# Kernel optimization log

Hardware: AMD Instinct MI355X
Metric: run time of the kernel (lower is better)

Reference implementation:

```python
import jax, jax.numpy as jnp
import numpy as np

B, S, H, G, DH = 2, 2048, 16, 4, 64
D = H * DH        # 1024
DKV = G * DH      # 256
SCALE = 1.0 / np.sqrt(DH).astype(np.float32)


def apply_rope(x, rope):
    # x: [..., S, DH]; rope: [2, S, DH] (rope[0]=cos, rope[1]=sin)
    xr = x.reshape(*x.shape[:-1], DH // 2, 2)
    x_rot = jnp.stack([-xr[..., 1], xr[..., 0]], axis=-1).reshape(x.shape)
    return x * rope[0] + x_rot * rope[1]


def setup_inputs() -> dict:
    key = jax.random.key(0)
    ks = jax.random.split(key, 5)
    X = jax.random.normal(ks[0], (B, S, D), dtype=jnp.float32)
    Wq = jax.random.normal(ks[1], (D, D), dtype=jnp.float32) / np.sqrt(D).astype(np.float32)
    Wk = jax.random.normal(ks[2], (DKV, D), dtype=jnp.float32) / np.sqrt(D).astype(np.float32)
    Wv = jax.random.normal(ks[3], (DKV, D), dtype=jnp.float32) / np.sqrt(D).astype(np.float32)
    Wo = jax.random.normal(ks[4], (D, D), dtype=jnp.float32) / np.sqrt(D).astype(np.float32)
    # standard RoPE angles, interleaved (pairs (0,1),(2,3),...)
    pos = jnp.arange(S, dtype=jnp.float32)
    inv_freq = 1.0 / (10000.0 ** (jnp.arange(0, DH, 2, dtype=jnp.float32) / DH))
    ang = pos[:, None] * inv_freq[None, :]          # [S, DH/2]
    ang = jnp.repeat(ang, 2, axis=-1)               # [S, DH]
    rope = jnp.stack([jnp.cos(ang), jnp.sin(ang)])  # [2, S, DH]
    causal = jnp.tril(jnp.ones((S, S), dtype=bool))
    return {"X": X, "Wq": Wq, "Wk": Wk, "Wv": Wv, "Wo": Wo, "rope": rope, "causal": causal}


def reference(X, Wq, Wk, Wv, Wo, rope, causal):
    # QKV projections (torch Linear: y = x @ W.T)
    Q = (X @ Wq.T).reshape(B, S, H, DH).transpose(0, 2, 1, 3)   # [B,H,S,DH]
    K = (X @ Wk.T).reshape(B, S, G, DH).transpose(0, 2, 1, 3)   # [B,G,S,DH]
    V = (X @ Wv.T).reshape(B, S, G, DH).transpose(0, 2, 1, 3)   # [B,G,S,DH]
    Q = apply_rope(Q, rope)
    K = apply_rope(K, rope)
    # GQA: repeat KV heads (repeat_interleave semantics)
    K = jnp.repeat(K, H // G, axis=1)                            # [B,H,S,DH]
    V = jnp.repeat(V, H // G, axis=1)
    scores = SCALE * jnp.einsum('bhqd,bhkd->bhqk', Q, K)         # [B,H,S,S]
    scores = jnp.where(causal, scores, -jnp.inf)
    A = jax.nn.softmax(scores, axis=-1)
    Y = jnp.einsum('bhqk,bhkd->bhqd', A, V)                      # [B,H,S,DH]
    Y = Y.transpose(0, 2, 1, 3).reshape(B, S, D)
    return Y @ Wo.T
```

## Files before the change

### kernel.cpp

```cpp
#include <hip/hip_runtime.h>
#include <hip/hip_bf16.h>

#define B_   2
#define S_   2048
#define H_   16
#define G_   4
#define DH_  64
#define D_   1024
#define DKV_ 256
#define SCALE_ 0.125f
#define LDQK_ 1280

using short8  = __attribute__((ext_vector_type(8))) short;
using floatx4 = __attribute__((ext_vector_type(4))) float;
typedef unsigned short ushort_t;

__device__ __forceinline__ ushort_t f2bf(float f) {
    union { float f; unsigned u; } v; v.f = f;
    unsigned r = v.u + 0x7fffu + ((v.u >> 16) & 1u);
    return (ushort_t)(r >> 16);
}
__device__ __forceinline__ unsigned cvt_pk_bf16(float lo, float hi) {
    unsigned r;
    asm("v_cvt_pk_bf16_f32 %0, %1, %2" : "=v"(r) : "v"(lo), "v"(hi));
    return r;
}

__device__ __forceinline__ void gload16(const ushort_t* g, ushort_t* l) {
    __builtin_amdgcn_global_load_lds(
        (const __attribute__((address_space(1))) void*)g,
        (__attribute__((address_space(3))) void*)l, 16, 0, 0);
}

__global__ void pack_all(const float* __restrict__ X,  const float* __restrict__ Wq,
                         const float* __restrict__ Wk, const float* __restrict__ Wv,
                         const float* __restrict__ Wo, ushort_t* __restrict__ dst) {
    const int X4  = B_ * S_ * D_ / 4;
    const int QW4 = D_ * D_ / 4;
    const int KW4 = DKV_ * D_ / 4;
    int i = blockIdx.x * blockDim.x + threadIdx.x;
    const float* src; int off;
    if (i < X4)                        { src = X;  off = i; }
    else if (i < X4 + QW4)             { src = Wq; off = i - X4; }
    else if (i < X4 + QW4 + KW4)       { src = Wk; off = i - X4 - QW4; }
    else if (i < X4 + QW4 + 2 * KW4)   { src = Wv; off = i - X4 - QW4 - KW4; }
    else                               { src = Wo; off = i - X4 - QW4 - 2 * KW4; }
    float4 v = reinterpret_cast<const float4*>(src)[off];
    ushort4 o;
    o.x = f2bf(v.x); o.y = f2bf(v.y); o.z = f2bf(v.z); o.w = f2bf(v.w);
    reinterpret_cast<ushort4*>(dst)[i] = o;
}

__global__ __launch_bounds__(256)
void gemm_all(int mode,
              const ushort_t* __restrict__ Xb,  const ushort_t* __restrict__ Wqkb,
              const ushort_t* __restrict__ Wvb, const ushort_t* __restrict__ Wob,
              ushort_t* __restrict__ QKb, ushort_t* __restrict__ Vtb,
              const ushort_t* __restrict__ Yb, float* __restrict__ Cout,
              const float* __restrict__ rope, float qscale)
{
    __shared__ __align__(16) ushort_t Asm[2][128 * 64];
    __shared__ __align__(16) ushort_t Bsm[2][128 * 64];

    const ushort_t *Aorig, *Borig;
    ushort_t* Cb = nullptr; float* Cf = nullptr;
    int m0, n0, ldc, epi;
    if (mode == 1) {
        m0 = blockIdx.x * 128; n0 = blockIdx.y * 128;
        Aorig = Yb; Borig = Wob; Cf = Cout; ldc = D_; epi = 1;
    } else {
        const int bx = blockIdx.x;
        if (bx < 320) {
            m0 = (bx / 10) * 128; n0 = (bx % 10) * 128;
            Aorig = Xb; Borig = Wqkb; Cb = QKb; ldc = LDQK_; epi = 2;
        } else {
            const int idx = bx - 320, b = idx >> 5, rem = idx & 31;
            m0 = (rem >> 4) * 128; n0 = (rem & 15) * 128;
            Aorig = Wvb; Borig = Xb + (long)b * S_ * D_;
            Cb = Vtb + (long)b * DKV_ * S_; ldc = S_; epi = 0;
        }
    }

    const int tid = threadIdx.x, l = tid & 63, w = tid >> 6;
    const int wr = (w >> 1) * 64, wc = (w & 1) * 64;
    const int lr = l & 15, lkb = l >> 4;

    const int srow = w * 8 + (l >> 3);
    const int scol = ((l & 7) ^ ((l >> 3) & 7)) * 8;
    const ushort_t* Ast = Aorig + (long)(m0 + srow) * D_ + scol;
    const ushort_t* Bst = Borig + (long)(n0 + srow) * D_ + scol;

#define GSTAGE(buf, kt)                                                    \
    {                                                                      \
        _Pragma("unroll")                                                  \
        for (int rr = 0; rr < 4; ++rr) {                                   \
            gload16(Ast + (long)rr * 32 * D_ + (kt), &Asm[buf][w * 512 + rr * 2048]); \
            gload16(Bst + (long)rr * 32 * D_ + (kt), &Bsm[buf][w * 512 + rr * 2048]); \
        }                                                                  \
    }

    floatx4 acc[4][4] = {};
    const int xr = (lr & 7) << 4;
    GSTAGE(0, 0);
    for (int i = 0; i < 16; ++i) {
        const int cur = i & 1;
        if (i < 15) {
            GSTAGE(cur ^ 1, (i + 1) * 64);
            asm volatile("s_waitcnt vmcnt(8)" ::: "memory");
        } else {
            asm volatile("s_waitcnt vmcnt(0)" ::: "memory");
        }
        __builtin_amdgcn_s_barrier();

#pragma unroll
        for (int ks = 0; ks < 2; ++ks) {
            short8 a[4], bb[4];
#pragma unroll
            for (int ii = 0; ii < 4; ++ii) {
                const int row = wr + ii * 16 + lr;
                a[ii] = *(const short8*)&Asm[cur][(row * 128 + ((ks * 64 + lkb * 16) ^ xr)) >> 1];
            }
#pragma unroll
            for (int j = 0; j < 4; ++j) {
                const int row = wc + j * 16 + lr;
                bb[j] = *(const short8*)&Bsm[cur][(row * 128 + ((ks * 64 + lkb * 16) ^ xr)) >> 1];
            }
            __builtin_amdgcn_s_setprio(1);
#pragma unroll
            for (int ii = 0; ii < 4; ++ii)
#pragma unroll
                for (int j = 0; j < 4; ++j)
                    acc[ii][j] = __builtin_amdgcn_mfma_f32_16x16x32_bf16(a[ii], bb[j], acc[ii][j], 0, 0, 0);
            __builtin_amdgcn_s_setprio(0);
        }
        __builtin_amdgcn_s_barrier();
    }
#undef GSTAGE

    const int rrow = lkb * 4;
#pragma unroll
    for (int i = 0; i < 4; ++i) {
#pragma unroll
        for (int j = 0; j < 4; ++j) {
#pragma unroll
            for (int r = 0; r < 4; ++r) {
                const int row = m0 + wr + i * 16 + rrow + r;
                const int col = n0 + wc + j * 16 + lr;
                if (epi == 1) {
                    Cf[(long)row * ldc + col] = acc[i][j][r];
                } else if (epi == 0) {
                    Cb[(long)row * ldc + col] = f2bf(acc[i][j][r]);
                } else {
                    const float v  = acc[i][j][r];
                    const float pv = __shfl_xor(v, 1);
                    const int   s  = row & (S_ - 1);
                    const int   d  = col & (DH_ - 1);
                    const float cc = rope[s * DH_ + d];
                    const float sn = rope[S_ * DH_ + s * DH_ + d];
                    float res = (lr & 1) ? (v * cc + pv * sn) : (v * cc - pv * sn);
                    res *= (col < D_) ? qscale : 1.0f;
                    Cb[(long)row * ldc + col] = f2bf(res);
                }
            }
        }
    }
}

__global__ __launch_bounds__(256)
void attn_kernel(const ushort_t* __restrict__ QK, const ushort_t* __restrict__ Vt,
                 ushort_t* __restrict__ Y)
{
    __shared__ __align__(16) ushort_t Kt [2][64 * 64];
    __shared__ __align__(16) ushort_t Vts[2][64 * 64];

    const int tid = threadIdx.x;
    const int l   = tid & 63;
    const int w   = tid >> 6;
    const int lr  = l & 15, lkb = l >> 4, lk = lkb * 8;
    const int bx = blockIdx.x, h = blockIdx.y, b = blockIdx.z;
    const int g   = h >> 2;

    const int sr  = l >> 3;
    const int sce = ((l & 7) ^ sr) * 8;
    const ushort_t* Ksrc = QK + (long)b * S_ * LDQK_ + D_ + g * DH_ + sce;
    const ushort_t* Vsrc = Vt + (long)(b * G_ + g) * DH_ * S_ + sce;

    short8 vones;
#pragma unroll
    for (int j = 0; j < 8; ++j) vones[j] = (short)0x3F80;

#define STAGE(buf, t_)                                                          \
    {                                                                           \
        const int kvb_ = (t_) * 64;                                             \
        _Pragma("unroll")                                                       \
        for (int c = 0; c < 2; ++c) {                                           \
            const int rloc = c * 32 + w * 8 + sr;                               \
            const int krow = (rloc & 0x23) | ((rloc & 0x0C) << 1) | ((rloc & 0x10) >> 2); \
            gload16(Ksrc + (long)(kvb_ + krow) * LDQK_, &Kt[buf][c * 2048 + w * 512]); \
            gload16(Vsrc + (long)rloc * S_ + kvb_,     &Vts[buf][c * 2048 + w * 512]); \
        }                                                                       \
    }

    for (int pass = 0; pass < 2; ++pass) {
        const int qt = pass == 0 ? (S_ / 64 - 1 - bx) : bx;
        const int qrow0 = qt * 64 + w * 16;

        const ushort_t* Qp = QK + ((long)b * S_ + qrow0 + lr) * LDQK_ + h * DH_ + lk;
        const short8 bq0 = *(const short8*)(Qp);
        const short8 bq1 = *(const short8*)(Qp + 32);

        floatx4 o[4] = {};
        floatx4 osum = {};
        const int nt = qt + 1;

        STAGE(0, 0);
        asm volatile("s_waitcnt vmcnt(0)" ::: "memory");
        __builtin_amdgcn_s_barrier();

        for (int t = 0; t < nt; ++t) {
            const int cur = t & 1;
            if (t + 1 < nt) STAGE(cur ^ 1, t + 1);

            floatx4 sacc[4] = {};
            __builtin_amdgcn_s_setprio(1);
#pragma unroll
            for (int cf = 0; cf < 4; ++cf) {
                const int row = cf * 16 + lr;
                const int xr  = (row & 7) << 4;
                const short8 ak0 = *(const short8*)&Kt[cur][(row * 128 + ((lkb * 16) ^ xr)) >> 1];
                const short8 ak1 = *(const short8*)&Kt[cur][(row * 128 + ((64 + lkb * 16) ^ xr)) >> 1];
                sacc[cf] = __builtin_amdgcn_mfma_f32_16x16x32_bf16(ak0, bq0, sacc[cf], 0, 0, 0);
                sacc[cf] = __builtin_amdgcn_mfma_f32_16x16x32_bf16(ak1, bq1, sacc[cf], 0, 0, 0);
            }
            __builtin_amdgcn_s_setprio(0);

            float p[16];
#pragma unroll
            for (int cf = 0; cf < 4; ++cf)
#pragma unroll
                for (int r = 0; r < 4; ++r)
                    p[cf * 4 + r] = sacc[cf][r];
            if (t == qt) {
                const int qg = qrow0 + lr;
#pragma unroll
                for (int cf = 0; cf < 4; ++cf) {
                    const int kvb0 = t * 64 + 32 * (cf >> 1) + 8 * lkb + 4 * (cf & 1);
#pragma unroll
                    for (int r = 0; r < 4; ++r)
                        if (kvb0 + r > qg) p[cf * 4 + r] = -3e38f;
                }
            }

#pragma unroll
            for (int i = 0; i < 16; ++i) p[i] = exp2f(p[i]);

#pragma unroll
            for (int ks = 0; ks < 2; ++ks) {
                union { unsigned u[4]; short8 s; } pa;
#pragma unroll
                for (int j = 0; j < 4; ++j)
                    pa.u[j] = cvt_pk_bf16(p[ks * 8 + 2 * j], p[ks * 8 + 2 * j + 1]);
                __builtin_amdgcn_s_setprio(1);
#pragma unroll
                for (int df = 0; df < 4; ++df) {
                    const int vrow = df * 16 + lr;
                    const int xr   = (vrow & 7) << 4;
                    const short8 bv = *(const short8*)&Vts[cur][(vrow * 128 + ((ks * 64 + lkb * 16) ^ xr)) >> 1];
                    o[df] = __builtin_amdgcn_mfma_f32_16x16x32_bf16(pa.s, bv, o[df], 0, 0, 0);
                }
                osum = __builtin_amdgcn_mfma_f32_16x16x32_bf16(pa.s, vones, osum, 0, 0, 0);
                __builtin_amdgcn_s_setprio(0);
            }

            asm volatile("s_waitcnt vmcnt(0)" ::: "memory");
            __builtin_amdgcn_s_barrier();
        }

#pragma unroll
        for (int r = 0; r < 4; ++r) {
            const float linv = 1.f / osum[r];
            const int row = qrow0 + lkb * 4 + r;
#pragma unroll
            for (int df = 0; df < 4; ++df)
                Y[((long)b * S_ + row) * D_ + h * DH_ + df * 16 + lr] = f2bf(o[df][r] * linv);
        }
    }
#undef STAGE
}

extern "C" void kernel_launch(void* const* d_in, const int* in_sizes, int n_in,
                              void* d_out, int out_size, void* d_ws, size_t ws_size,
                              hipStream_t stream) {
    const float* X    = (const float*)d_in[0];
    const float* Wq   = (const float*)d_in[1];
    const float* Wk   = (const float*)d_in[2];
    const float* Wv   = (const float*)d_in[3];
    const float* Wo   = (const float*)d_in[4];
    const float* rope = (const float*)d_in[5];
    float* out = (float*)d_out;

    char* ws = (char*)d_ws;
    size_t o = 0;
    ushort_t* Xb   = (ushort_t*)(ws + o); o += (size_t)B_ * S_ * D_ * 2;
    ushort_t* Wqkb = (ushort_t*)(ws + o); o += (size_t)LDQK_ * D_ * 2;
    ushort_t* Wvb  = (ushort_t*)(ws + o); o += (size_t)DKV_ * D_ * 2;
    ushort_t* Wob  = (ushort_t*)(ws + o); o += (size_t)D_ * D_ * 2;
    ushort_t* QKb  = (ushort_t*)(ws + o); o += (size_t)B_ * S_ * LDQK_ * 2;
    ushort_t* Vtb  = (ushort_t*)(ws + o); o += (size_t)B_ * G_ * DH_ * S_ * 2;
    ushort_t* Yb   = Xb;

    {
        int n4 = (B_ * S_ * D_ + 2 * D_ * D_ + 2 * DKV_ * D_) / 4;
        pack_all<<<(n4 + 255) / 256, 256, 0, stream>>>(X, Wq, Wk, Wv, Wo, Xb);
    }

    const float SC2 = SCALE_ * 1.44269504f;
    gemm_all<<<dim3(384, 1, 1), 256, 0, stream>>>(
        0, Xb, Wqkb, Wvb, Wob, QKb, Vtb, nullptr, nullptr, rope, SC2);

    attn_kernel<<<dim3(S_ / 128, H_, B_), 256, 0, stream>>>(QKb, Vtb, Yb);

    gemm_all<<<dim3(32, 8, 1), 256, 0, stream>>>(
        1, Xb, Wqkb, Wvb, Wob, QKb, Vtb, Yb, out, nullptr, 0.f);
}
```

Baseline: 113.2 us.

## Split causal attention KV range across two blocks and add combine kernel

The attention grid doubles. Each block now processes one KV half for each of two paired query tiles instead of the full KV range. Partial outputs are written unnormalized in bf16 along with per-row exp-sums, and a new combine kernel sums the two halves and normalizes them. The aim is more blocks and shorter per-block work to improve CU utilization and reduce tail effects, at the cost of an extra kernel launch, roughly 24 MB more global traffic, and bf16 rounding of unnormalized partials.

```diff
diff --git a/kernel.cpp b/kernel.cpp
--- a/kernel.cpp
+++ b/kernel.cpp
@@ -19,6 +19,10 @@
     union { float f; unsigned u; } v; v.f = f;
     unsigned r = v.u + 0x7fffu + ((v.u >> 16) & 1u);
     return (ushort_t)(r >> 16);
+}
+__device__ __forceinline__ float bf2f(ushort_t u) {
+    union { unsigned u; float f; } v; v.u = ((unsigned)u) << 16;
+    return v.f;
 }
 __device__ __forceinline__ unsigned cvt_pk_bf16(float lo, float hi) {
     unsigned r;
@@ -168,7 +172,8 @@
 
 __global__ __launch_bounds__(256)
 void attn_kernel(const ushort_t* __restrict__ QK, const ushort_t* __restrict__ Vt,
-                 ushort_t* __restrict__ Y)
+                 ushort_t* __restrict__ Y0, ushort_t* __restrict__ Y1,
+                 float* __restrict__ L0, float* __restrict__ L1)
 {
     __shared__ __align__(16) ushort_t Kt [2][64 * 64];
     __shared__ __align__(16) ushort_t Vts[2][64 * 64];
@@ -201,8 +206,12 @@
         }                                                                       \
     }
 
-    for (int pass = 0; pass < 2; ++pass) {
-        const int qt = pass == 0 ? (S_ / 64 - 1 - bx) : bx;
+    for (int seg = 0; seg < 2; ++seg) {
+        const int qt   = seg == 0 ? (S_ / 64 - 1 - bx) : bx;
+        const int half = seg == 0 ? 1 : 0;
+        const int split = (qt + 2) / 2;
+        const int t0 = half ? split : 0;
+        const int t1 = half ? qt + 1 : split;
         const int qrow0 = qt * 64 + w * 16;
 
         const ushort_t* Qp = QK + ((long)b * S_ + qrow0 + lr) * LDQK_ + h * DH_ + lk;
@@ -211,81 +220,103 @@
 
         floatx4 o[4] = {};
         floatx4 osum = {};
-        const int nt = qt + 1;
-
-        STAGE(0, 0);
-        asm volatile("s_waitcnt vmcnt(0)" ::: "memory");
-        __builtin_amdgcn_s_barrier();
-
-        for (int t = 0; t < nt; ++t) {
-            const int cur = t & 1;
-            if (t + 1 < nt) STAGE(cur ^ 1, t + 1);
-
-            floatx4 sacc[4] = {};
-            __builtin_amdgcn_s_setprio(1);
-#pragma unroll
-            for (int cf = 0; cf < 4; ++cf) {
-                const int row = cf * 16 + lr;
-                const int xr  = (row & 7) << 4;
-                const short8 ak0 = *(const short8*)&Kt[cur][(row * 128 + ((lkb * 16) ^ xr)) >> 1];
-                const short8 ak1 = *(const short8*)&Kt[cur][(row * 128 + ((64 + lkb * 16) ^ xr)) >> 1];
-                sacc[cf] = __builtin_amdgcn_mfma_f32_16x16x32_bf16(ak0, bq0, sacc[cf], 0, 0, 0);
-                sacc[cf] = __builtin_amdgcn_mfma_f32_16x16x32_bf16(ak1, bq1, sacc[cf], 0, 0, 0);
-            }
-            __builtin_amdgcn_s_setprio(0);
-
-            float p[16];
-#pragma unroll
-            for (int cf = 0; cf < 4; ++cf)
-#pragma unroll
-                for (int r = 0; r < 4; ++r)
-                    p[cf * 4 + r] = sacc[cf][r];
-            if (t == qt) {
-                const int qg = qrow0 + lr;
-#pragma unroll
-                for (int cf = 0; cf < 4; ++cf) {
-                    const int kvb0 = t * 64 + 32 * (cf >> 1) + 8 * lkb + 4 * (cf & 1);
-#pragma unroll
-                    for (int r = 0; r < 4; ++r)
-                        if (kvb0 + r > qg) p[cf * 4 + r] = -3e38f;
-                }
-            }
-
-#pragma unroll
-            for (int i = 0; i < 16; ++i) p[i] = exp2f(p[i]);
-
-#pragma unroll
-            for (int ks = 0; ks < 2; ++ks) {
-                union { unsigned u[4]; short8 s; } pa;
-#pragma unroll
-                for (int j = 0; j < 4; ++j)
-                    pa.u[j] = cvt_pk_bf16(p[ks * 8 + 2 * j], p[ks * 8 + 2 * j + 1]);
-                __builtin_amdgcn_s_setprio(1);
-#pragma unroll
-                for (int df = 0; df < 4; ++df) {
-                    const int vrow = df * 16 + lr;
-                    const int xr   = (vrow & 7) << 4;
-                    const short8 bv = *(const short8*)&Vts[cur][(vrow * 128 + ((ks * 64 + lkb * 16) ^ xr)) >> 1];
-                    o[df] = __builtin_amdgcn_mfma_f32_16x16x32_bf16(pa.s, bv, o[df], 0, 0, 0);
-                }
-                osum = __builtin_amdgcn_mfma_f32_16x16x32_bf16(pa.s, vones, osum, 0, 0, 0);
-                __builtin_amdgcn_s_setprio(0);
-            }
-
+
+        if (t1 > t0) {
+            STAGE(0, t0);
             asm volatile("s_waitcnt vmcnt(0)" ::: "memory");
             __builtin_amdgcn_s_barrier();
-        }
-
+
+            for (int t = t0; t < t1; ++t) {
+                const int cur = (t - t0) & 1;
+                if (t + 1 < t1) STAGE(cur ^ 1, t + 1);
+
+                floatx4 sacc[4] = {};
+                __builtin_amdgcn_s_setprio(1);
+#pragma unroll
+                for (int cf = 0; cf < 4; ++cf) {
+                    const int row = cf * 16 + lr;
+                    const int xr  = (row & 7) << 4;
+                    const short8 ak0 = *(const short8*)&Kt[cur][(row * 128 + ((lkb * 16) ^ xr)) >> 1];
+                    const short8 ak1 = *(const short8*)&Kt[cur][(row * 128 + ((64 + lkb * 16) ^ xr)) >> 1];
+                    sacc[cf] = __builtin_amdgcn_mfma_f32_16x16x32_bf16(ak0, bq0, sacc[cf], 0, 0, 0);
+                    sacc[cf] = __builtin_amdgcn_mfma_f32_16x16x32_bf16(ak1, bq1, sacc[cf], 0, 0, 0);
+                }
+                __builtin_amdgcn_s_setprio(0);
+
+                float p[16];
+#pragma unroll
+                for (int cf = 0; cf < 4; ++cf)
+#pragma unroll
+                    for (int r = 0; r < 4; ++r)
+                        p[cf * 4 + r] = sacc[cf][r];
+                if (t == qt) {
+                    const int qg = qrow0 + lr;
+#pragma unroll
+                    for (int cf = 0; cf < 4; ++cf) {
+                        const int kvb0 = t * 64 + 32 * (cf >> 1) + 8 * lkb + 4 * (cf & 1);
+#pragma unroll
+                        for (int r = 0; r < 4; ++r)
+                            if (kvb0 + r > qg) p[cf * 4 + r] = -3e38f;
+                    }
+                }
+
+#pragma unroll
+                for (int i = 0; i < 16; ++i) p[i] = exp2f(p[i]);
+
+#pragma unroll
+                for (int ks = 0; ks < 2; ++ks) {
+                    union { unsigned u[4]; short8 s; } pa;
+#pragma unroll
+                    for (int j = 0; j < 4; ++j)
+                        pa.u[j] = cvt_pk_bf16(p[ks * 8 + 2 * j], p[ks * 8 + 2 * j + 1]);
+                    __builtin_amdgcn_s_setprio(1);
+#pragma unroll
+                    for (int df = 0; df < 4; ++df) {
+                        const int vrow = df * 16 + lr;
+                        const int xr   = (vrow & 7) << 4;
+                        const short8 bv = *(const short8*)&Vts[cur][(vrow * 128 + ((ks * 64 + lkb * 16) ^ xr)) >> 1];
+                        o[df] = __builtin_amdgcn_mfma_f32_16x16x32_bf16(pa.s, bv, o[df], 0, 0, 0);
+                    }
+                    osum = __builtin_amdgcn_mfma_f32_16x16x32_bf16(pa.s, vones, osum, 0, 0, 0);
+                    __builtin_amdgcn_s_setprio(0);
+                }
+
+                asm volatile("s_waitcnt vmcnt(0)" ::: "memory");
+                __builtin_amdgcn_s_barrier();
+            }
+        }
+
+        ushort_t* Yp = half ? Y1 : Y0;
+        float*    Lp = half ? L1 : L0;
 #pragma unroll
         for (int r = 0; r < 4; ++r) {
-            const float linv = 1.f / osum[r];
             const int row = qrow0 + lkb * 4 + r;
 #pragma unroll
             for (int df = 0; df < 4; ++df)
-                Y[((long)b * S_ + row) * D_ + h * DH_ + df * 16 + lr] = f2bf(o[df][r] * linv);
+                Yp[((long)b * S_ + row) * D_ + h * DH_ + df * 16 + lr] = f2bf(o[df][r]);
+            if (lr == 0)
+                Lp[((long)b * S_ + row) * H_ + h] = osum[r];
         }
     }
 #undef STAGE
+}
+
+__global__ void combine_kernel(ushort_t* __restrict__ Y0, const ushort_t* __restrict__ Y1,
+                               const float* __restrict__ L0, const float* __restrict__ L1) {
+    const int i  = blockIdx.x * blockDim.x + threadIdx.x;
+    const int row = i >> 7;
+    const int h   = (i & 127) >> 3;
+    const float inv = 1.f / (L0[row * H_ + h] + L1[row * H_ + h]);
+    const short8 y0 = ((const short8*)Y0)[i];
+    const short8 y1 = ((const short8*)Y1)[i];
+    union { unsigned u[4]; short8 s; } o;
+#pragma unroll
+    for (int j = 0; j < 4; ++j) {
+        const float a = (bf2f((ushort_t)y0[2 * j])     + bf2f((ushort_t)y1[2 * j]))     * inv;
+        const float c = (bf2f((ushort_t)y0[2 * j + 1]) + bf2f((ushort_t)y1[2 * j + 1])) * inv;
+        o.u[j] = cvt_pk_bf16(a, c);
+    }
+    ((short8*)Y0)[i] = o.s;
 }
 
 extern "C" void kernel_launch(void* const* d_in, const int* in_sizes, int n_in,
@@ -307,7 +338,10 @@
     ushort_t* Wob  = (ushort_t*)(ws + o); o += (size_t)D_ * D_ * 2;
     ushort_t* QKb  = (ushort_t*)(ws + o); o += (size_t)B_ * S_ * LDQK_ * 2;
     ushort_t* Vtb  = (ushort_t*)(ws + o); o += (size_t)B_ * G_ * DH_ * S_ * 2;
-    ushort_t* Yb   = Xb;
+    ushort_t* Y1b  = (ushort_t*)(ws + o); o += (size_t)B_ * S_ * D_ * 2;
+    float*    L0   = (float*)(ws + o);    o += (size_t)B_ * S_ * H_ * 4;
+    float*    L1   = (float*)(ws + o);    o += (size_t)B_ * S_ * H_ * 4;
+    ushort_t* Y0   = Xb;
 
     {
         int n4 = (B_ * S_ * D_ + 2 * D_ * D_ + 2 * DKV_ * D_) / 4;
@@ -318,8 +352,13 @@
     gemm_all<<<dim3(384, 1, 1), 256, 0, stream>>>(
         0, Xb, Wqkb, Wvb, Wob, QKb, Vtb, nullptr, nullptr, rope, SC2);
 
-    attn_kernel<<<dim3(S_ / 128, H_, B_), 256, 0, stream>>>(QKb, Vtb, Yb);
+    attn_kernel<<<dim3(32, H_, B_), 256, 0, stream>>>(QKb, Vtb, Y0, Y1b, L0, L1);
+
+    {
+        int nthr = B_ * S_ * D_ / 8;
+        combine_kernel<<<nthr / 256, 256, 0, stream>>>(Y0, Y1b, L0, L1);
+    }
 
     gemm_all<<<dim3(32, 8, 1), 256, 0, stream>>>(
-        1, Xb, Wqkb, Wvb, Wob, QKb, Vtb, Yb, out, nullptr, 0.f);
-}
+        1, Xb, Wqkb, Wvb, Wob, QKb, Vtb, Y0, out, nullptr, 0.f);
+}
```

After: 115.6 us. 1.02x slower.
